# Optimization experiments

Measured on AMD Instinct MI355X. Metric: run time of the kernel, lower is better.

Reference implementation:

```python
import jax, jax.numpy as jnp
import numpy as np

N_NODES = 1_000_000
N_EDGES = 32_000_000
N_SPECIES = 100
A0 = 0.5291772105638411
KE = 14.399645351950548


def softplus_inverse(x):
    return x + jnp.log(-jnp.expm1(-x))


def setup_inputs() -> dict:
    key = jax.random.key(0)
    k1, k2, k3, k4, k5 = jax.random.split(key, 5)
    node_species = jax.random.randint(k1, (N_NODES,), 0, N_SPECIES, dtype=jnp.int32)
    distances = jax.random.uniform(k2, (N_EDGES,), dtype=jnp.float32)
    cutoffs = jax.random.uniform(k3, (N_EDGES,), dtype=jnp.float32)
    senders = jax.random.randint(k4, (N_EDGES,), 0, N_NODES, dtype=jnp.int32)
    receivers = jax.random.randint(k5, (N_EDGES,), 0, N_NODES, dtype=jnp.int32)
    index_to_z = jnp.arange(1, N_SPECIES + 1, dtype=jnp.int32)
    # learned params (raw, softplus applied in reference) at their constant inits
    a_raw = softplus_inverse(jnp.array([3.2, 0.9423, 0.4028, 0.2016], dtype=jnp.float32))
    c_raw = softplus_inverse(jnp.array([0.1818, 0.5099, 0.2802, 0.02817], dtype=jnp.float32))
    p_raw = jnp.full((1,), softplus_inverse(jnp.float32(0.23)), dtype=jnp.float32)
    d_raw = jnp.full((1,), softplus_inverse(jnp.float32(1.0 / (0.8854 * A0))), dtype=jnp.float32)
    return {
        'node_species': node_species, 'distances': distances, 'cutoffs': cutoffs,
        'senders': senders, 'receivers': receivers, 'index_to_z': index_to_z,
        'a_raw': a_raw, 'c_raw': c_raw, 'p_raw': p_raw, 'd_raw': d_raw,
    }


def reference(node_species, distances, cutoffs, senders, receivers, index_to_z,
              a_raw, c_raw, p_raw, d_raw):
    a = jax.nn.softplus(a_raw)                       # [4]
    c = jax.nn.softplus(c_raw)
    c = c / jnp.sum(c)                               # [4]
    p = jax.nn.softplus(p_raw)                       # [1]
    d = jax.nn.softplus(d_raw)                       # [1]

    z = index_to_z[node_species]                     # [N]
    z_i = z[receivers].astype(jnp.float32)           # [E]
    z_j = z[senders].astype(jnp.float32)             # [E]

    x = KE * cutoffs * z_i * z_j / (distances + 1e-08)              # [E]
    rzd = distances * (jnp.power(z_i, p) + jnp.power(z_j, p)) * d   # [E]
    y = jnp.sum(c * jnp.exp(-a * rzd[:, None]), axis=-1)            # [E]

    scaled_d = distances / 1.5
    sigma_d = jnp.exp(-1.0 / jnp.where(scaled_d > 1e-08, scaled_d, 1e-08))
    sigma_1_d = jnp.exp(-1.0 / jnp.where(1 - scaled_d > 1e-08, 1 - scaled_d, 1e-08))
    w = sigma_1_d / (sigma_1_d + sigma_d)

    energy_rep = w * x * y / 2                                       # [E]
    return jax.ops.segment_sum(energy_rep, receivers, num_segments=node_species.shape[0])
```

## Files before the change

kernel.cpp:

```cpp
#include <hip/hip_runtime.h>

#define SPECIES_CAP 128
#define WS_A   0
#define WS_C   4
#define WS_ZF  16
#define WS_ZPD (16 + SPECIES_CAP)

#define NB       256
#define RSHIFT   12
#define RNODES   4096
#define NSUB     4
#define CNT_STRIDE 16

#define ITER     16
#define CHUNK    (ITER / 4)
#define TILE     (256 * ITER)

#define PARAMS_OFF 0
#define CNT_OFF    4096
#define CNT_BYTES  ((size_t)NB * NSUB * CNT_STRIDE * 4)
#define PAIRS_OFF  (CNT_OFF + CNT_BYTES)

__global__ void zbl_setup(const float* __restrict__ a_raw,
                          const float* __restrict__ c_raw,
                          const float* __restrict__ p_raw,
                          const float* __restrict__ d_raw,
                          const int* __restrict__ index_to_z,
                          int n_species,
                          float* __restrict__ params)
{
    __shared__ float s_p, s_d;
    int t = threadIdx.x;
    if (t == 0) {
        float a[4], c[4];
        float csum = 0.0f;
        for (int i = 0; i < 4; ++i) {
            a[i] = log1pf(expf(a_raw[i]));
            c[i] = log1pf(expf(c_raw[i]));
            csum += c[i];
        }
        for (int i = 0; i < 4; ++i) {
            params[WS_A + i] = a[i];
            params[WS_C + i] = c[i] / csum;
        }
        float p = log1pf(expf(p_raw[0]));
        float d = log1pf(expf(d_raw[0]));
        params[8] = p;
        params[9] = d;
        s_p = p;
        s_d = d;
    }
    __syncthreads();
    float p = s_p, d = s_d;
    for (int s = t; s < n_species && s < SPECIES_CAP; s += blockDim.x) {
        float z = (float)index_to_z[s];
        params[WS_ZF + s]  = z;
        params[WS_ZPD + s] = powf(z, p) * d;
    }
}

__device__ __forceinline__ float zbl_energy(
    float dist, float cut, int snd, int rcv,
    const int* __restrict__ node_species,
    const float* s_zf, const float* s_zpd,
    const float* s_a, const float* s_c)
{
    int si = node_species[rcv];
    int sj = node_species[snd];
    float zi = s_zf[si];
    float zj = s_zf[sj];
    float x = cut * zi * zj / (dist + 1e-8f);
    float rzd = dist * (s_zpd[si] + s_zpd[sj]);
    float y = s_c[0] * __expf(-s_a[0] * rzd)
            + s_c[1] * __expf(-s_a[1] * rzd)
            + s_c[2] * __expf(-s_a[2] * rzd)
            + s_c[3] * __expf(-s_a[3] * rzd);
    float sd = dist * (1.0f / 1.5f);
    float u1 = (sd > 1e-8f) ? sd : 1e-8f;
    float u2 = ((1.0f - sd) > 1e-8f) ? (1.0f - sd) : 1e-8f;
    float e_d  = __expf(-1.0f / u1);
    float e_1d = __expf(-1.0f / u2);
    float w = e_1d / (e_1d + e_d);
    return 7.199822675975274f * w * x * y;
}

__global__ __launch_bounds__(256) void zbl_bin_kernel(
    const float* __restrict__ distances,
    const float* __restrict__ cutoffs,
    const int* __restrict__ senders,
    const int* __restrict__ receivers,
    const int* __restrict__ node_species,
    const float* __restrict__ params,
    unsigned* __restrict__ cnt,
    uint2* __restrict__ pairs,
    int cap,
    float* __restrict__ out,
    int E)
{
    __shared__ float s_zf[SPECIES_CAP];
    __shared__ float s_zpd[SPECIES_CAP];
    __shared__ float s_a[4];
    __shared__ float s_c[4];
    __shared__ unsigned h_cnt[NB];
    __shared__ unsigned h_base[NB];
    int t = threadIdx.x;
    if (t < 4)              s_a[t]     = params[WS_A + t];
    else if (t < 8)         s_c[t - 4] = params[WS_C + (t - 4)];
    for (int s = t; s < SPECIES_CAP; s += 256) {
        s_zf[s]  = params[WS_ZF + s];
        s_zpd[s] = params[WS_ZPD + s];
    }
    for (int s = t; s < NB; s += 256) h_cnt[s] = 0u;
    __syncthreads();

    float en[ITER];
    int   rc[ITER];
    int sub = blockIdx.x & (NSUB - 1);

#pragma unroll
    for (int c = 0; c < CHUNK; ++c) {
        int vbase = (blockIdx.x * (256 * CHUNK) + c * 256 + t) * 4;
        if (vbase + 4 <= E) {
            float4 d4 = *(const float4*)(distances + vbase);
            float4 c4 = *(const float4*)(cutoffs + vbase);
            int4   s4 = *(const int4*)(senders + vbase);
            int4   r4 = *(const int4*)(receivers + vbase);
            int   sn[4] = { s4.x, s4.y, s4.z, s4.w };
            int   rr[4] = { r4.x, r4.y, r4.z, r4.w };
            float dd[4] = { d4.x, d4.y, d4.z, d4.w };
            float cc[4] = { c4.x, c4.y, c4.z, c4.w };
#pragma unroll
            for (int k = 0; k < 4; ++k) {
                rc[c * 4 + k] = rr[k];
                en[c * 4 + k] = zbl_energy(dd[k], cc[k], sn[k], rr[k],
                                           node_species, s_zf, s_zpd, s_a, s_c);
            }
#pragma unroll
            for (int k = 0; k < 4; ++k)
                atomicAdd(&h_cnt[((unsigned)rr[k]) >> RSHIFT], 1u);
        } else {
#pragma unroll
            for (int k = 0; k < 4; ++k) {
                int e = vbase + k;
                if (e < E) {
                    int rcv = receivers[e];
                    rc[c * 4 + k] = rcv;
                    en[c * 4 + k] = zbl_energy(distances[e], cutoffs[e],
                                               senders[e], rcv,
                                               node_species, s_zf, s_zpd,
                                               s_a, s_c);
                    atomicAdd(&h_cnt[((unsigned)rcv) >> RSHIFT], 1u);
                } else {
                    rc[c * 4 + k] = -1;
                }
            }
        }
    }
    __syncthreads();

    {
        unsigned n = h_cnt[t];
        h_base[t] = n ? atomicAdd(&cnt[(t * NSUB + sub) * CNT_STRIDE], n) : 0u;
        h_cnt[t] = 0u;
    }
    __syncthreads();

#pragma unroll
    for (int k = 0; k < ITER; ++k) {
        if (rc[k] >= 0) {
            unsigned b = ((unsigned)rc[k]) >> RSHIFT;
            unsigned pos = h_base[b] + atomicAdd(&h_cnt[b], 1u);
            if (pos < (unsigned)cap)
                pairs[(size_t)(b * NSUB + sub) * cap + pos] =
                    make_uint2((unsigned)rc[k], __float_as_uint(en[k]));
            else
                unsafeAtomicAdd(out + rc[k], en[k]);
        }
    }
}

__global__ __launch_bounds__(1024) void zbl_reduce_kernel(
    const unsigned* __restrict__ cnt,
    const uint2* __restrict__ pairs,
    int cap,
    float* __restrict__ out,
    int n_nodes)
{
    __shared__ float acc[RNODES];
    int b = blockIdx.x;
    int t = threadIdx.x;
    for (int i = t; i < RNODES; i += 1024) acc[i] = 0.0f;
    __syncthreads();

    for (int sub = 0; sub < NSUB; ++sub) {
        int bs = b * NSUB + sub;
        int entries = min((int)cnt[bs * CNT_STRIDE], cap);
        const uint2* pb = pairs + (size_t)bs * cap;
        const uint4* pb4 = (const uint4*)pb;
        int n2 = entries >> 1;
        for (int j = t; j < n2; j += 1024) {
            uint4 q = pb4[j];
            atomicAdd(&acc[q.x & (RNODES - 1)], __uint_as_float(q.y));
            atomicAdd(&acc[q.z & (RNODES - 1)], __uint_as_float(q.w));
        }
        if ((entries & 1) && t == 0) {
            uint2 pr = pb[entries - 1];
            atomicAdd(&acc[pr.x & (RNODES - 1)], __uint_as_float(pr.y));
        }
    }
    __syncthreads();

    int nbase = b << RSHIFT;
    int nmax  = n_nodes - nbase;
    if (nmax <= 0) return;
    if (nmax >= RNODES) {
        float4* o4 = (float4*)(out + nbase);
        const float4* a4 = (const float4*)acc;
        for (int i = t; i < RNODES / 4; i += 1024) {
            float4 v = a4[i];
            float4 o = o4[i];
            o.x += v.x; o.y += v.y; o.z += v.z; o.w += v.w;
            o4[i] = o;
        }
    } else {
        for (int i = t; i < nmax; i += 1024)
            out[nbase + i] += acc[i];
    }
}

__global__ __launch_bounds__(256) void zbl_direct_kernel(
    const float* __restrict__ distances,
    const float* __restrict__ cutoffs,
    const int* __restrict__ senders,
    const int* __restrict__ receivers,
    const int* __restrict__ node_species,
    const float* __restrict__ params,
    float* __restrict__ out,
    int E)
{
    __shared__ float s_zf[SPECIES_CAP];
    __shared__ float s_zpd[SPECIES_CAP];
    __shared__ float s_a[4];
    __shared__ float s_c[4];
    int t = threadIdx.x;
    if (t < 4)              s_a[t]     = params[WS_A + t];
    else if (t < 8)         s_c[t - 4] = params[WS_C + (t - 4)];
    for (int s = t; s < SPECIES_CAP; s += blockDim.x) {
        s_zf[s]  = params[WS_ZF + s];
        s_zpd[s] = params[WS_ZPD + s];
    }
    __syncthreads();
    int base = (blockIdx.x * 256 + t) * 4;
    int lim = min(base + 4, E);
    for (int e = base; e < lim; ++e) {
        int rcv = receivers[e];
        float en = zbl_energy(distances[e], cutoffs[e], senders[e], rcv,
                              node_species, s_zf, s_zpd, s_a, s_c);
        unsafeAtomicAdd(out + rcv, en);
    }
}

extern "C" void kernel_launch(void* const* d_in, const int* in_sizes, int n_in,
                              void* d_out, int out_size, void* d_ws, size_t ws_size,
                              hipStream_t stream)
{
    const int*   node_species = (const int*)d_in[0];
    const float* distances    = (const float*)d_in[1];
    const float* cutoffs      = (const float*)d_in[2];
    const int*   senders      = (const int*)d_in[3];
    const int*   receivers    = (const int*)d_in[4];
    const int*   index_to_z   = (const int*)d_in[5];
    const float* a_raw        = (const float*)d_in[6];
    const float* c_raw        = (const float*)d_in[7];
    const float* p_raw        = (const float*)d_in[8];
    const float* d_raw        = (const float*)d_in[9];

    int E         = in_sizes[1];
    int n_species = in_sizes[5];
    int n_nodes   = in_sizes[0];
    float*    out    = (float*)d_out;
    float*    params = (float*)((char*)d_ws + PARAMS_OFF);
    unsigned* cnt    = (unsigned*)((char*)d_ws + CNT_OFF);
    uint2*    pairs  = (uint2*)((char*)d_ws + PAIRS_OFF);

    size_t avail = (ws_size > PAIRS_OFF) ? (ws_size - PAIRS_OFF) : 0;
    long long cap_ll = (long long)(avail / ((size_t)NB * NSUB * sizeof(uint2)));
    int want = E / (NB * NSUB) + E / (NB * NSUB * 4) + 1024;
    int cap = (int)((cap_ll < (long long)want) ? cap_ll : (long long)want);
    cap &= ~1;

    hipMemsetAsync(d_out, 0, (size_t)out_size * sizeof(float), stream);
    zbl_setup<<<1, 128, 0, stream>>>(a_raw, c_raw, p_raw, d_raw,
                                     index_to_z, n_species, params);

    if (cap >= 4096) {
        hipMemsetAsync(cnt, 0, CNT_BYTES, stream);
        int blocks = (E + TILE - 1) / TILE;
        zbl_bin_kernel<<<blocks, 256, 0, stream>>>(
            distances, cutoffs, senders, receivers, node_species,
            params, cnt, pairs, cap, out, E);
        zbl_reduce_kernel<<<NB, 1024, 0, stream>>>(
            cnt, pairs, cap, out, n_nodes);
    } else {
        int blocks = ((E + 3) / 4 + 255) / 256;
        zbl_direct_kernel<<<blocks, 256, 0, stream>>>(
            distances, cutoffs, senders, receivers, node_species,
            params, out, E);
    }
}
```

Before: 1.118 ms.

## Stage binned pairs in shared memory for coalesced writes; split reduce per sub-bin

The bin kernel now records each edge's local rank within its bucket during the histogram pass. A block-wide prefix scan then gives bucket offsets, and (receiver, energy) pairs are sorted into a 32KB shared-memory staging buffer. Pairs are written to global memory as contiguous runs per bucket instead of scattered per-thread writes. The reduce kernel launches one 256-thread block per (bucket, sub) pair rather than one 1024-thread block per bucket, and merges its results into the output with atomics; this adds more parallelism but more global atomics and more LDS use in the bin kernel, which may lower occupancy.

```diff
diff --git a/kernel.cpp b/kernel.cpp
--- a/kernel.cpp
+++ b/kernel.cpp
@@ -102,7 +102,11 @@
     __shared__ float s_a[4];
     __shared__ float s_c[4];
     __shared__ unsigned h_cnt[NB];
-    __shared__ unsigned h_base[NB];
+    __shared__ unsigned h_lbase[NB];
+    __shared__ unsigned h_gbase[NB];
+    __shared__ unsigned wtot[4];
+    __shared__ unsigned s_total;
+    __shared__ uint2 stg[TILE];
     int t = threadIdx.x;
     if (t < 4)              s_a[t]     = params[WS_A + t];
     else if (t < 8)         s_c[t - 4] = params[WS_C + (t - 4)];
@@ -110,11 +114,12 @@
         s_zf[s]  = params[WS_ZF + s];
         s_zpd[s] = params[WS_ZPD + s];
     }
-    for (int s = t; s < NB; s += 256) h_cnt[s] = 0u;
-    __syncthreads();
-
-    float en[ITER];
-    int   rc[ITER];
+    h_cnt[t] = 0u;
+    __syncthreads();
+
+    float    en[ITER];
+    unsigned pk[ITER];
+    unsigned vmask = 0u;
     int sub = blockIdx.x & (NSUB - 1);
 
 #pragma unroll
@@ -130,28 +135,30 @@
             float dd[4] = { d4.x, d4.y, d4.z, d4.w };
             float cc[4] = { c4.x, c4.y, c4.z, c4.w };
 #pragma unroll
-            for (int k = 0; k < 4; ++k) {
-                rc[c * 4 + k] = rr[k];
+            for (int k = 0; k < 4; ++k)
                 en[c * 4 + k] = zbl_energy(dd[k], cc[k], sn[k], rr[k],
                                            node_species, s_zf, s_zpd, s_a, s_c);
+#pragma unroll
+            for (int k = 0; k < 4; ++k) {
+                unsigned b  = ((unsigned)rr[k]) >> RSHIFT;
+                unsigned rk = atomicAdd(&h_cnt[b], 1u);
+                pk[c * 4 + k] = (rk << 20) | (unsigned)rr[k];
+                vmask |= 1u << (c * 4 + k);
             }
-#pragma unroll
-            for (int k = 0; k < 4; ++k)
-                atomicAdd(&h_cnt[((unsigned)rr[k]) >> RSHIFT], 1u);
         } else {
 #pragma unroll
             for (int k = 0; k < 4; ++k) {
                 int e = vbase + k;
                 if (e < E) {
                     int rcv = receivers[e];
-                    rc[c * 4 + k] = rcv;
                     en[c * 4 + k] = zbl_energy(distances[e], cutoffs[e],
                                                senders[e], rcv,
                                                node_species, s_zf, s_zpd,
                                                s_a, s_c);
-                    atomicAdd(&h_cnt[((unsigned)rcv) >> RSHIFT], 1u);
-                } else {
-                    rc[c * 4 + k] = -1;
+                    unsigned b  = ((unsigned)rcv) >> RSHIFT;
+                    unsigned rk = atomicAdd(&h_cnt[b], 1u);
+                    pk[c * 4 + k] = (rk << 20) | (unsigned)rcv;
+                    vmask |= 1u << (c * 4 + k);
                 }
             }
         }
@@ -159,27 +166,54 @@
     __syncthreads();
 
     {
-        unsigned n = h_cnt[t];
-        h_base[t] = n ? atomicAdd(&cnt[(t * NSUB + sub) * CNT_STRIDE], n) : 0u;
-        h_cnt[t] = 0u;
+        unsigned orig = h_cnt[t];
+        unsigned v = orig;
+        int lane = t & 63;
+#pragma unroll
+        for (int d = 1; d < 64; d <<= 1) {
+            unsigned nv = __shfl_up(v, d, 64);
+            if (lane >= d) v += nv;
+        }
+        if (lane == 63) wtot[t >> 6] = v;
+        __syncthreads();
+        unsigned off = 0;
+        int wid = t >> 6;
+#pragma unroll
+        for (int w = 0; w < 3; ++w)
+            if (w < wid) off += wtot[w];
+        unsigned incl = off + v;
+        h_lbase[t] = incl - orig;
+        h_gbase[t] = orig
+            ? atomicAdd(&cnt[(t * NSUB + sub) * CNT_STRIDE], orig) : 0u;
+        if (t == 255) s_total = incl;
     }
     __syncthreads();
 
 #pragma unroll
     for (int k = 0; k < ITER; ++k) {
-        if (rc[k] >= 0) {
-            unsigned b = ((unsigned)rc[k]) >> RSHIFT;
-            unsigned pos = h_base[b] + atomicAdd(&h_cnt[b], 1u);
-            if (pos < (unsigned)cap)
-                pairs[(size_t)(b * NSUB + sub) * cap + pos] =
-                    make_uint2((unsigned)rc[k], __float_as_uint(en[k]));
-            else
-                unsafeAtomicAdd(out + rc[k], en[k]);
-        }
-    }
-}
-
-__global__ __launch_bounds__(1024) void zbl_reduce_kernel(
+        if ((vmask >> k) & 1u) {
+            unsigned u   = pk[k];
+            unsigned rcv = u & 0xFFFFFu;
+            unsigned rk  = u >> 20;
+            unsigned b   = rcv >> RSHIFT;
+            stg[h_lbase[b] + rk] = make_uint2(rcv, __float_as_uint(en[k]));
+        }
+    }
+    __syncthreads();
+
+    unsigned total = s_total;
+    for (unsigned i = t; i < total; i += 256) {
+        uint2 q = stg[i];
+        unsigned b   = q.x >> RSHIFT;
+        unsigned pos = h_gbase[b] + (i - h_lbase[b]);
+        if (pos < (unsigned)cap)
+            pairs[(size_t)(b * NSUB + sub) * cap + pos] = q;
+        else
+            unsafeAtomicAdd(out + q.x, __uint_as_float(q.y));
+    }
+}
+
+__global__ __launch_bounds__(256) void zbl_reduce_kernel(
     const unsigned* __restrict__ cnt,
     const uint2* __restrict__ pairs,
     int cap,
@@ -187,44 +221,34 @@
     int n_nodes)
 {
     __shared__ float acc[RNODES];
-    int b = blockIdx.x;
-    int t = threadIdx.x;
-    for (int i = t; i < RNODES; i += 1024) acc[i] = 0.0f;
-    __syncthreads();
-
-    for (int sub = 0; sub < NSUB; ++sub) {
-        int bs = b * NSUB + sub;
-        int entries = min((int)cnt[bs * CNT_STRIDE], cap);
-        const uint2* pb = pairs + (size_t)bs * cap;
-        const uint4* pb4 = (const uint4*)pb;
-        int n2 = entries >> 1;
-        for (int j = t; j < n2; j += 1024) {
-            uint4 q = pb4[j];
-            atomicAdd(&acc[q.x & (RNODES - 1)], __uint_as_float(q.y));
-            atomicAdd(&acc[q.z & (RNODES - 1)], __uint_as_float(q.w));
-        }
-        if ((entries & 1) && t == 0) {
-            uint2 pr = pb[entries - 1];
-            atomicAdd(&acc[pr.x & (RNODES - 1)], __uint_as_float(pr.y));
-        }
+    int bs = blockIdx.x;
+    int b  = bs / NSUB;
+    int t  = threadIdx.x;
+    for (int i = t; i < RNODES; i += 256) acc[i] = 0.0f;
+    __syncthreads();
+
+    int entries = min((int)cnt[bs * CNT_STRIDE], cap);
+    const uint2* pb  = pairs + (size_t)bs * cap;
+    const uint4* pb4 = (const uint4*)pb;
+    int n2 = entries >> 1;
+    for (int j = t; j < n2; j += 256) {
+        uint4 q = pb4[j];
+        atomicAdd(&acc[q.x & (RNODES - 1)], __uint_as_float(q.y));
+        atomicAdd(&acc[q.z & (RNODES - 1)], __uint_as_float(q.w));
+    }
+    if ((entries & 1) && t == 0) {
+        uint2 pr = pb[entries - 1];
+        atomicAdd(&acc[pr.x & (RNODES - 1)], __uint_as_float(pr.y));
     }
     __syncthreads();
 
     int nbase = b << RSHIFT;
     int nmax  = n_nodes - nbase;
     if (nmax <= 0) return;
-    if (nmax >= RNODES) {
-        float4* o4 = (float4*)(out + nbase);
-        const float4* a4 = (const float4*)acc;
-        for (int i = t; i < RNODES / 4; i += 1024) {
-            float4 v = a4[i];
-            float4 o = o4[i];
-            o.x += v.x; o.y += v.y; o.z += v.z; o.w += v.w;
-            o4[i] = o;
-        }
-    } else {
-        for (int i = t; i < nmax; i += 1024)
-            out[nbase + i] += acc[i];
+    int lim = (nmax < RNODES) ? nmax : RNODES;
+    for (int i = t; i < lim; i += 256) {
+        float v = acc[i];
+        if (v != 0.0f) unsafeAtomicAdd(out + nbase + i, v);
     }
 }
 
@@ -293,13 +317,13 @@
     zbl_setup<<<1, 128, 0, stream>>>(a_raw, c_raw, p_raw, d_raw,
                                      index_to_z, n_species, params);
 
-    if (cap >= 4096) {
+    if (cap >= 4096 && n_nodes <= (1 << 20)) {
         hipMemsetAsync(cnt, 0, CNT_BYTES, stream);
         int blocks = (E + TILE - 1) / TILE;
         zbl_bin_kernel<<<blocks, 256, 0, stream>>>(
             distances, cutoffs, senders, receivers, node_species,
             params, cnt, pairs, cap, out, E);
-        zbl_reduce_kernel<<<NB, 1024, 0, stream>>>(
+        zbl_reduce_kernel<<<NB * NSUB, 256, 0, stream>>>(
             cnt, pairs, cap, out, n_nodes);
     } else {
         int blocks = ((E + 3) / 4 + 255) / 256;
```

Result: faster. 1.035 ms (-7.4%).
